# Performance work log

Measured on AMD Instinct MI355X. Metric: run time of the kernel, lower is better.

Reference implementation:

```python
import jax, jax.numpy as jnp
import numpy as np

EMB_W, COMMIT_W, ENT_W = 1.0, 0.25, 0.1  # loss weights from init_kwargs


def setup_inputs() -> dict:
    key = jax.random.key(0)
    k1, k2 = jax.random.split(key)
    B, H, W, D, K = 32, 32, 32, 64, 1024
    inputs = jax.random.normal(k1, (B, H, W, D), dtype=jnp.float32)
    # keras RandomUniform default: U(-0.05, 0.05)
    codebook = jax.random.uniform(k2, (K, D), dtype=jnp.float32, minval=-0.05, maxval=0.05)
    return {"inputs": inputs, "codebook": codebook}


def reference(inputs, codebook):
    # inputs: [B,H,W,D], codebook: [K,D]
    D = inputs.shape[-1]
    x = inputs.reshape(-1, D)  # [N,D]
    dist = (
        jnp.sum(x * x, axis=-1, keepdims=True)
        - 2.0 * (x @ codebook.T)
        + jnp.sum(codebook * codebook, axis=-1)
    )  # [N,K]
    tokens = jnp.argmin(dist, axis=-1)  # [N]
    emb = codebook[tokens].reshape(inputs.shape)  # [B,H,W,D]

    embedding_loss = EMB_W * jnp.mean((jax.lax.stop_gradient(emb) - inputs) ** 2)
    commitment_loss = COMMIT_W * jnp.mean((emb - jax.lax.stop_gradient(inputs)) ** 2)
    # 'entropy' loss as written in call(): mean over codebook of per-code min distance
    entropy_loss = ENT_W * jnp.mean(jnp.min(dist, axis=0))
    loss = embedding_loss + commitment_loss + entropy_loss

    # training=True path: straight-through estimator
    out = inputs + jax.lax.stop_gradient(emb - inputs)
    return out, loss
```

## Files before the change

kernel.cpp:

```cpp
#include <hip/hip_runtime.h>
#include <math.h>

#define NROWS 32768
#define NCODE 1024
#define AMB_CAP 8192
#define GAP_THRESH 1.5e-4f

typedef __attribute__((ext_vector_type(8))) short bf16x8;
typedef __attribute__((ext_vector_type(4))) float f32x4;

__device__ __forceinline__ unsigned short bf16_rne(float f) {
    unsigned u = __float_as_uint(f);
    unsigned r = u + 0x7FFFu + ((u >> 16) & 1u);
    return (unsigned short)(r >> 16);
}

__global__ __launch_bounds__(64) void vq_prep(
    const float* __restrict__ cb, float* __restrict__ cn4,
    unsigned* __restrict__ minK, unsigned* __restrict__ counter,
    float* __restrict__ gsumsq, unsigned* __restrict__ ticket,
    unsigned short* __restrict__ wsB)
{
    int c = blockIdx.x * 64 + threadIdx.x;
    if (c == 0) { *counter = 0u; *gsumsq = 0.f; *ticket = 0u; }
    float v[64];
    const float4* src = (const float4*)(cb + (size_t)c * 64);
    float s = 0.f;
    #pragma unroll
    for (int i = 0; i < 16; i++) {
        float4 t = src[i];
        v[i*4+0] = t.x; v[i*4+1] = t.y; v[i*4+2] = t.z; v[i*4+3] = t.w;
        s += t.x*t.x + t.y*t.y + t.z*t.z + t.w*t.w;
    }
    cn4[c] = s + 4.0f;
    minK[c] = 0x7F800000u;
    int cc = c >> 6, ct = (c >> 4) & 3, cl = c & 15;
    #pragma unroll
    for (int q = 0; q < 4; q++) {
        int half = q & 1, lo = q >> 1;
        #pragma unroll
        for (int g = 0; g < 4; g++) {
            unsigned short u8[8] __attribute__((aligned(16)));
            #pragma unroll
            for (int j = 0; j < 8; j++) {
                float f = -2.0f * v[half*32 + g*8 + j];
                unsigned short h = bf16_rne(f);
                if (lo) h = bf16_rne(f - __uint_as_float((unsigned)h << 16));
                u8[j] = h;
            }
            size_t off = (size_t)cc * 8192 + ct * 2048 + q * 512 + (g * 16 + cl) * 8;
            *(uint4*)(wsB + off) = *(const uint4*)u8;
        }
    }
}

__global__ __launch_bounds__(512, 4) void vq_main(
    const float* __restrict__ x, const float* __restrict__ cb,
    const unsigned short* __restrict__ wsB, const float* __restrict__ cn4,
    float* __restrict__ out, unsigned* __restrict__ minK,
    unsigned* __restrict__ counter, int* __restrict__ amb,
    float* __restrict__ gsumsq)
{
    __shared__ float    cn4L[1024];
    __shared__ unsigned scrE[1024];
    __shared__ float mD1[128], mD2[128];
    __shared__ int   mI1[128];
    __shared__ int   tokS[64];
    __shared__ float redS[8];

    const int tid = threadIdx.x;
    const int lane = tid & 63;
    const int wi = tid >> 6;
    const int g = wi >> 1;
    const int h = wi & 1;
    const int ln15 = lane & 15;
    const int q = lane >> 4;
    const int row0 = blockIdx.x * 64;

    cn4L[tid]       = cn4[tid];
    cn4L[512 + tid] = cn4[512 + tid];
    scrE[tid]       = 0x7F800000u;
    scrE[512 + tid] = 0x7F800000u;

    bf16x8 Ah0, Ah1, Al0, Al1;
    float xnm4[4];
    {
        const float* xr = x + (size_t)(row0 + g*16 + ln15) * 64 + q * 8;
        float4 f0 = *(const float4*)xr;
        float4 f1 = *(const float4*)(xr + 4);
        float4 f2 = *(const float4*)(xr + 32);
        float4 f3 = *(const float4*)(xr + 36);
        float fa[8] = {f0.x,f0.y,f0.z,f0.w,f1.x,f1.y,f1.z,f1.w};
        float fb[8] = {f2.x,f2.y,f2.z,f2.w,f3.x,f3.y,f3.z,f3.w};
        unsigned short hh8[8] __attribute__((aligned(16)));
        unsigned short ll8[8] __attribute__((aligned(16)));
        unsigned short h28[8] __attribute__((aligned(16)));
        unsigned short l28[8] __attribute__((aligned(16)));
        float ss = 0.f;
        #pragma unroll
        for (int j = 0; j < 8; j++) {
            ss += fa[j]*fa[j] + fb[j]*fb[j];
            unsigned short hh = bf16_rne(fa[j]);
            hh8[j] = hh; ll8[j] = bf16_rne(fa[j] - __uint_as_float((unsigned)hh << 16));
            hh = bf16_rne(fb[j]);
            h28[j] = hh; l28[j] = bf16_rne(fb[j] - __uint_as_float((unsigned)hh << 16));
        }
        Ah0 = *(const bf16x8*)hh8; Al0 = *(const bf16x8*)ll8;
        Ah1 = *(const bf16x8*)h28; Al1 = *(const bf16x8*)l28;
        ss += __shfl_xor(ss, 16);
        ss += __shfl_xor(ss, 32);
        #pragma unroll
        for (int r = 0; r < 4; r++)
            xnm4[r] = __shfl(ss, (q << 2) | r, 64) - 4.0f;
    }
    __syncthreads();

    float d1[4], d2[4];
    int   i1[4];
    #pragma unroll
    for (int r = 0; r < 4; r++) { d1[r] = INFINITY; d2[r] = INFINITY; i1[r] = 0; }

    const char* wsQ = (const char*)wsB + (size_t)h * 131072 + lane * 16;

#define PF(S, T_) { const char* tb_ = wsQ + (T_) * 4096;                        \
        S##h0 = *(const bf16x8*)(tb_);                                          \
        S##h1 = *(const bf16x8*)(tb_ + 1024);                                   \
        S##l0 = *(const bf16x8*)(tb_ + 2048);                                   \
        S##l1 = *(const bf16x8*)(tb_ + 3072); }

#define COMP(S, T_) {                                                           \
        const int kid_ = h*512 + (T_)*16 + ln15;                                \
        const float cn4v_ = cn4L[kid_];                                         \
        f32x4 a0_ = {cn4v_, cn4v_, cn4v_, cn4v_};                               \
        a0_ = __builtin_amdgcn_mfma_f32_16x16x32_bf16(Ah0, S##h0, a0_, 0, 0, 0);\
        a0_ = __builtin_amdgcn_mfma_f32_16x16x32_bf16(Ah1, S##h1, a0_, 0, 0, 0);\
        a0_ = __builtin_amdgcn_mfma_f32_16x16x32_bf16(Ah0, S##l0, a0_, 0, 0, 0);\
        a0_ = __builtin_amdgcn_mfma_f32_16x16x32_bf16(Ah1, S##l1, a0_, 0, 0, 0);\
        a0_ = __builtin_amdgcn_mfma_f32_16x16x32_bf16(Al0, S##h0, a0_, 0, 0, 0);\
        a0_ = __builtin_amdgcn_mfma_f32_16x16x32_bf16(Al1, S##h1, a0_, 0, 0, 0);\
        float cm_ = INFINITY;                                                   \
        _Pragma("unroll")                                                       \
        for (int r_ = 0; r_ < 4; r_++) {                                        \
            float wv = a0_[r_];                                                 \
            d2[r_] = fminf(fmaxf(wv, d1[r_]), d2[r_]);                          \
            bool lt = wv < d1[r_];                                              \
            i1[r_] = lt ? kid_ : i1[r_];                                        \
            d1[r_] = fminf(wv, d1[r_]);                                         \
            cm_ = fminf(cm_, wv + xnm4[r_]);                                    \
        }                                                                       \
        cm_ = fminf(cm_, __shfl_xor(cm_, 16));                                  \
        cm_ = fminf(cm_, __shfl_xor(cm_, 32));                                  \
        if (q == ((T_) & 3)) atomicMin(&scrE[kid_], __float_as_uint(cm_)); }

    bf16x8 SAh0,SAh1,SAl0,SAl1, SBh0,SBh1,SBl0,SBl1,
           SCh0,SCh1,SCl0,SCl1, SDh0,SDh1,SDl0,SDl1;
    PF(SA, 0); PF(SB, 1); PF(SC, 2);
    for (int tb = 0; tb < 28; tb += 4) {
        PF(SD, tb+3); COMP(SA, tb+0);
        PF(SA, tb+4); COMP(SB, tb+1);
        PF(SB, tb+5); COMP(SC, tb+2);
        PF(SC, tb+6); COMP(SD, tb+3);
    }
    PF(SD, 31);
    COMP(SA, 28); COMP(SB, 29); COMP(SC, 30); COMP(SD, 31);

#undef PF
#undef COMP

    #pragma unroll
    for (int d = 1; d < 16; d <<= 1) {
        #pragma unroll
        for (int r = 0; r < 4; r++) {
            float od1 = __shfl_xor(d1[r], d);
            int   oi1 = __shfl_xor(i1[r], d);
            float od2 = __shfl_xor(d2[r], d);
            bool take = (od1 < d1[r]) || (od1 == d1[r] && oi1 < i1[r]);
            float loser = take ? d1[r] : od1;
            d2[r] = fminf(fminf(d2[r], od2), loser);
            d1[r] = take ? od1 : d1[r];
            i1[r] = take ? oi1 : i1[r];
        }
    }
    if (ln15 == 0) {
        #pragma unroll
        for (int r = 0; r < 4; r++) {
            int idx = (g*16 + q*4 + r) * 2 + h;
            mD1[idx] = d1[r]; mI1[idx] = i1[r]; mD2[idx] = d2[r];
        }
    }
    __syncthreads();

    if (tid < 64) {
        float a1 = mD1[tid*2],   b1 = mD1[tid*2+1];
        int   ai = mI1[tid*2],   bi = mI1[tid*2+1];
        float a2 = mD2[tid*2],   b2 = mD2[tid*2+1];
        bool ta = (a1 < b1) || (a1 == b1 && ai < bi);
        float D1 = ta ? a1 : b1;
        int   I1 = ta ? ai : bi;
        float D2 = ta ? fminf(a2, b1) : fminf(b2, a1);
        tokS[tid] = I1;
        if (D2 - D1 < GAP_THRESH) {
            unsigned idx = atomicAdd(counter, 1u);
            if (idx < AMB_CAP) { amb[2*idx] = row0 + tid; amb[2*idx+1] = I1; }
        }
    }

    {
        unsigned u0 = scrE[tid];
        if (u0 < minK[tid]) atomicMin(&minK[tid], u0);
        unsigned u1 = scrE[512 + tid];
        if (u1 < minK[512 + tid]) atomicMin(&minK[512 + tid], u1);
    }
    __syncthreads();

    {
        float acc2 = 0.f;
        #pragma unroll
        for (int uu = 0; uu < 2; uu++) {
            int u = uu*512 + tid;
            int row = u >> 4, c4 = u & 15;
            int tok = tokS[row];
            float4 c = ((const float4*)(cb + (size_t)tok*64))[c4];
            float4 xx = ((const float4*)(x + (size_t)(row0 + row)*64))[c4];
            ((float4*)(out + (size_t)(row0 + row)*64))[c4] = c;
            float dx = c.x-xx.x, dy = c.y-xx.y, dz = c.z-xx.z, dw = c.w-xx.w;
            acc2 += dx*dx + dy*dy + dz*dz + dw*dw;
        }
        #pragma unroll
        for (int o = 32; o > 0; o >>= 1) acc2 += __shfl_down(acc2, o);
        if (lane == 0) redS[wi] = acc2;
        __syncthreads();
        if (tid == 0) {
            float t = 0.f;
            #pragma unroll
            for (int w = 0; w < 8; w++) t += redS[w];
            atomicAdd(gsumsq, t);
        }
    }
}

__global__ __launch_bounds__(256) void vq_tail(
    const float* __restrict__ x, const float* __restrict__ cb,
    float* __restrict__ out, const unsigned* __restrict__ counter,
    const int* __restrict__ amb, float* __restrict__ gsumsq,
    unsigned* __restrict__ ticket, const unsigned* __restrict__ minK,
    float* __restrict__ out_loss)
{
    __shared__ __align__(16) float cbS[16384];
    __shared__ double xs[64];
    __shared__ double bd[256];
    __shared__ int    bi[256];
    __shared__ unsigned lastS;
    __shared__ float redS[4];

    const int tid = threadIdx.x;

    unsigned cnt = *counter; if (cnt > AMB_CAP) cnt = AMB_CAP;
    for (unsigned i = blockIdx.x; i < cnt; i += gridDim.x) {
        int row = amb[2*i], oldk = amb[2*i+1];
        __syncthreads();
        if (tid < 64) xs[tid] = (double)x[(size_t)row*64 + tid];
        __syncthreads();
        double xn = 0.0;
        #pragma unroll 8
        for (int d = 0; d < 64; d++) xn += xs[d]*xs[d];
        double best = INFINITY; int bk = 1 << 30;
        for (int b = 0; b < 4; b++) {
            __syncthreads();
            #pragma unroll
            for (int k = 0; k < 16; k++)
                ((float4*)cbS)[k*256 + tid] = ((const float4*)cb)[b*4096 + k*256 + tid];
            __syncthreads();
            int kcode = b*256 + tid;
            const int t6 = tid & 63;
            double dot = 0.0, cn2 = 0.0;
            #pragma unroll 8
            for (int dd = 0; dd < 64; dd++) {
                int d = (dd + t6) & 63;
                double cv = (double)cbS[tid*64 + d];
                dot = fma(xs[d], cv, dot);
                cn2 = fma(cv, cv, cn2);
            }
            double dist = (xn - 2.0*dot) + cn2;
            if (dist < best || (dist == best && kcode < bk)) { best = dist; bk = kcode; }
        }
        bd[tid] = best; bi[tid] = bk;
        __syncthreads();
        for (int s = 128; s > 0; s >>= 1) {
            if (tid < s) {
                double od = bd[tid+s]; int ok = bi[tid+s];
                if (od < bd[tid] || (od == bd[tid] && ok < bi[tid])) { bd[tid] = od; bi[tid] = ok; }
            }
            __syncthreads();
        }
        int bestk = bi[0];
        if (bestk != oldk) {
            double part = 0.0;
            if (tid < 64) {
                float cn = cb[(size_t)bestk*64 + tid];
                float co = cb[(size_t)oldk*64 + tid];
                out[(size_t)row*64 + tid] = cn;
                double dn = (double)cn - xs[tid];
                double dl = (double)co - xs[tid];
                part = dn*dn - dl*dl;
            }
            __syncthreads();
            bd[tid] = part;
            __syncthreads();
            for (int s = 128; s > 0; s >>= 1) {
                if (tid < s) bd[tid] += bd[tid+s];
                __syncthreads();
            }
            if (tid == 0) atomicAdd(gsumsq, (float)bd[0]);
        }
    }

    __syncthreads();
    if (tid == 0) {
        __threadfence();
        lastS = (atomicAdd(ticket, 1u) == 63u) ? 1u : 0u;
    }
    __syncthreads();
    if (lastS) {
        __threadfence();
        float s = 0.f;
        #pragma unroll
        for (int jj = 0; jj < 4; jj++)
            s += __uint_as_float(minK[jj*256 + tid]);
        #pragma unroll
        for (int o = 32; o > 0; o >>= 1) s += __shfl_down(s, o);
        if ((tid & 63) == 0) redS[tid >> 6] = s;
        __syncthreads();
        if (tid == 0) {
            float gs = atomicAdd(gsumsq, 0.0f);
            float tot = redS[0] + redS[1] + redS[2] + redS[3];
            out_loss[0] = 1.25f * (gs / 2097152.0f) + 0.1f * (tot / 1024.0f);
        }
    }
}

extern "C" void kernel_launch(void* const* d_in, const int* in_sizes, int n_in,
                              void* d_out, int out_size, void* d_ws, size_t ws_size,
                              hipStream_t stream) {
    const float* x  = (const float*)d_in[0];
    const float* cb = (const float*)d_in[1];
    float* out = (float*)d_out;

    char* ws = (char*)d_ws;
    unsigned*       counter = (unsigned*)ws;
    float*          gsumsq  = (float*)(ws + 4);
    unsigned*       ticket  = (unsigned*)(ws + 8);
    float*          cn4     = (float*)(ws + 1024);
    unsigned*       minK    = (unsigned*)(ws + 8192);
    int*            amb     = (int*)(ws + 16384);
    unsigned short* wsB     = (unsigned short*)(ws + 131072);

    vq_prep<<<16,  64,  0, stream>>>(cb, cn4, minK, counter, gsumsq, ticket, wsB);
    vq_main<<<512, 512, 0, stream>>>(x, cb, wsB, cn4, out, minK, counter, amb, gsumsq);
    vq_tail<<<64,  256, 0, stream>>>(x, cb, out, counter, amb, gsumsq, ticket, minK,
                                     out + 2097152);
}
```

Before: 124.2 us.

## Hand-schedule codebook tile loads with inline asm and explicit vmcnt waits

Replaces the compiler-scheduled four-deep register prefetch of codebook tiles with a three-buffer rotation. Each tile is fetched by inline global_load_dwordx4 asm, and the code waits with explicit s_waitcnt vmcnt plus sched barriers. This keeps loads in flight across the MFMA compute and lowers register pressure. It also drops the cross-quarter shuffle reduction of the per-code min and has every lane issue the atomicMin directly. That removes two shuffles per tile but raises the number of atomics four-fold. The manual waitcnt counting must exactly match the outstanding loads, or correctness suffers.

```diff
diff --git a/kernel.cpp b/kernel.cpp
--- a/kernel.cpp
+++ b/kernel.cpp
@@ -122,22 +122,28 @@
 
     const char* wsQ = (const char*)wsB + (size_t)h * 131072 + lane * 16;
 
-#define PF(S, T_) { const char* tb_ = wsQ + (T_) * 4096;                        \
-        S##h0 = *(const bf16x8*)(tb_);                                          \
-        S##h1 = *(const bf16x8*)(tb_ + 1024);                                   \
-        S##l0 = *(const bf16x8*)(tb_ + 2048);                                   \
-        S##l1 = *(const bf16x8*)(tb_ + 3072); }
-
-#define COMP(S, T_) {                                                           \
+#define PFT(B0, B1, B2, B3, T_) {                                               \
+        unsigned long long a_ = (unsigned long long)(wsQ + (size_t)(T_) * 4096);\
+        asm volatile("global_load_dwordx4 %0, %4, off\n\t"                      \
+                     "global_load_dwordx4 %1, %4, off offset:1024\n\t"          \
+                     "global_load_dwordx4 %2, %4, off offset:2048\n\t"          \
+                     "global_load_dwordx4 %3, %4, off offset:3072"              \
+                     : "=&v"(B0), "=&v"(B1), "=&v"(B2), "=&v"(B3)               \
+                     : "v"(a_) : "memory"); }
+
+#define WCNT(N_) { asm volatile("s_waitcnt vmcnt(" #N_ ")" ::: "memory");       \
+                   __builtin_amdgcn_sched_barrier(0); }
+
+#define COMPT(B0, B1, B2, B3, T_) {                                             \
         const int kid_ = h*512 + (T_)*16 + ln15;                                \
         const float cn4v_ = cn4L[kid_];                                         \
         f32x4 a0_ = {cn4v_, cn4v_, cn4v_, cn4v_};                               \
-        a0_ = __builtin_amdgcn_mfma_f32_16x16x32_bf16(Ah0, S##h0, a0_, 0, 0, 0);\
-        a0_ = __builtin_amdgcn_mfma_f32_16x16x32_bf16(Ah1, S##h1, a0_, 0, 0, 0);\
-        a0_ = __builtin_amdgcn_mfma_f32_16x16x32_bf16(Ah0, S##l0, a0_, 0, 0, 0);\
-        a0_ = __builtin_amdgcn_mfma_f32_16x16x32_bf16(Ah1, S##l1, a0_, 0, 0, 0);\
-        a0_ = __builtin_amdgcn_mfma_f32_16x16x32_bf16(Al0, S##h0, a0_, 0, 0, 0);\
-        a0_ = __builtin_amdgcn_mfma_f32_16x16x32_bf16(Al1, S##h1, a0_, 0, 0, 0);\
+        a0_ = __builtin_amdgcn_mfma_f32_16x16x32_bf16(Ah0, B0, a0_, 0, 0, 0);   \
+        a0_ = __builtin_amdgcn_mfma_f32_16x16x32_bf16(Ah1, B1, a0_, 0, 0, 0);   \
+        a0_ = __builtin_amdgcn_mfma_f32_16x16x32_bf16(Ah0, B2, a0_, 0, 0, 0);   \
+        a0_ = __builtin_amdgcn_mfma_f32_16x16x32_bf16(Ah1, B3, a0_, 0, 0, 0);   \
+        a0_ = __builtin_amdgcn_mfma_f32_16x16x32_bf16(Al0, B0, a0_, 0, 0, 0);   \
+        a0_ = __builtin_amdgcn_mfma_f32_16x16x32_bf16(Al1, B1, a0_, 0, 0, 0);   \
         float cm_ = INFINITY;                                                   \
         _Pragma("unroll")                                                       \
         for (int r_ = 0; r_ < 4; r_++) {                                        \
@@ -148,24 +154,23 @@
             d1[r_] = fminf(wv, d1[r_]);                                         \
             cm_ = fminf(cm_, wv + xnm4[r_]);                                    \
         }                                                                       \
-        cm_ = fminf(cm_, __shfl_xor(cm_, 16));                                  \
-        cm_ = fminf(cm_, __shfl_xor(cm_, 32));                                  \
-        if (q == ((T_) & 3)) atomicMin(&scrE[kid_], __float_as_uint(cm_)); }
-
-    bf16x8 SAh0,SAh1,SAl0,SAl1, SBh0,SBh1,SBl0,SBl1,
-           SCh0,SCh1,SCl0,SCl1, SDh0,SDh1,SDl0,SDl1;
-    PF(SA, 0); PF(SB, 1); PF(SC, 2);
-    for (int tb = 0; tb < 28; tb += 4) {
-        PF(SD, tb+3); COMP(SA, tb+0);
-        PF(SA, tb+4); COMP(SB, tb+1);
-        PF(SB, tb+5); COMP(SC, tb+2);
-        PF(SC, tb+6); COMP(SD, tb+3);
-    }
-    PF(SD, 31);
-    COMP(SA, 28); COMP(SB, 29); COMP(SC, 30); COMP(SD, 31);
-
-#undef PF
-#undef COMP
+        atomicMin(&scrE[kid_], __float_as_uint(cm_)); }
+
+    bf16x8 Ab0, Ab1, Ab2, Ab3, Bb0, Bb1, Bb2, Bb3, Cb0, Cb1, Cb2, Cb3;
+    PFT(Ab0, Ab1, Ab2, Ab3, 0);
+    PFT(Bb0, Bb1, Bb2, Bb3, 1);
+    for (int i = 0; i < 10; i++) {
+        const int t0 = 3 * i;
+        PFT(Cb0, Cb1, Cb2, Cb3, t0 + 2); WCNT(8); COMPT(Ab0, Ab1, Ab2, Ab3, t0);
+        PFT(Ab0, Ab1, Ab2, Ab3, t0 + 3); WCNT(8); COMPT(Bb0, Bb1, Bb2, Bb3, t0 + 1);
+        PFT(Bb0, Bb1, Bb2, Bb3, t0 + 4); WCNT(8); COMPT(Cb0, Cb1, Cb2, Cb3, t0 + 2);
+    }
+    WCNT(4); COMPT(Ab0, Ab1, Ab2, Ab3, 30);
+    WCNT(0); COMPT(Bb0, Bb1, Bb2, Bb3, 31);
+
+#undef PFT
+#undef WCNT
+#undef COMPT
 
     #pragma unroll
     for (int d = 1; d < 16; d <<= 1) {
```

Result: faster. 115.2 us (-7.2%).
